# Performance work log

Hardware: AMD Instinct MI355X
Metric: run time of the kernel (lower is better)

## Reference

```python
import jax, jax.numpy as jnp
import numpy as np
import math

N_ENT = 200000
N_USERS = 100000
N_FACTORS = 4
N_REL = 26
CH = 64
N_EDGES = 1000000
NNZ = 1000000
KG_HEADS = 2


def scatter_softmax(scores, seg, num_segments):
    # numerically-stable softmax over groups defined by seg (per-head softmax)
    m = jax.ops.segment_max(scores, seg, num_segments=num_segments)
    m = jnp.where(jnp.isfinite(m), m, 0.0)
    e = jnp.exp(scores - m[seg])
    d = jax.ops.segment_sum(e, seg, num_segments=num_segments)
    return e / d[seg]


def setup_inputs() -> dict:
    key = jax.random.key(0)
    ks = jax.random.split(key, 11)
    return {
        "entity_emb": jax.random.normal(ks[0], (N_ENT, CH), dtype=jnp.float32) * 0.1,
        "user_emb": jax.random.normal(ks[1], (N_USERS, CH), dtype=jnp.float32) * 0.1,
        "latent_emb": jax.random.normal(ks[2], (N_FACTORS, CH), dtype=jnp.float32) * 0.1,
        "edge_index": jax.random.randint(ks[3], (2, N_EDGES), 0, N_ENT),
        "edge_type": jax.random.randint(ks[4], (N_EDGES,), 1, N_REL),  # in [1, N_REL-1]
        "ui_rows": jax.random.randint(ks[5], (NNZ,), 0, N_USERS),
        "ui_cols": jax.random.randint(ks[6], (NNZ,), 0, N_ENT),
        "ui_vals": jax.random.uniform(ks[7], (NNZ,), dtype=jnp.float32),
        "weight": jax.random.normal(ks[8], (N_REL - 1, CH), dtype=jnp.float32) * 0.1,
        "disen_weight_att": jax.random.normal(ks[9], (N_FACTORS, N_REL - 1), dtype=jnp.float32) * 0.1,
        "kg_W_r": jax.random.normal(ks[10], (CH, CH), dtype=jnp.float32) * (1.0 / math.sqrt(CH)),
    }


def reference(entity_emb, user_emb, latent_emb, edge_index, edge_type,
              ui_rows, ui_cols, ui_vals, weight, disen_weight_att, kg_W_r):
    head, tail = edge_index[0], edge_index[1]
    d_k = CH // KG_HEADS

    # --- Invariant_Capture.relation_aware_att ---
    rel_emb = weight[edge_type - 1]            # [E, C] gather
    h_emb = entity_emb[head]                   # [E, C] gather
    q = (h_emb @ kg_W_r).reshape(-1, KG_HEADS, d_k)
    k = (rel_emb @ kg_W_r).reshape(-1, KG_HEADS, d_k)
    score_r = ((q * k).sum(-1) / math.sqrt(d_k)).mean(-1)   # [E]
    rel_attn = scatter_softmax(score_r, head, N_ENT)

    # --- Invariant_Capture.kg_inv_capture ---
    t_emb = entity_emb[tail]                   # [E, C] gather
    r_emb = rel_emb * rel_attn[:, None]
    # bmm(cat(h,r), cat(t,r)^T) == h.t + r.r per edge
    score_trip = (h_emb * t_emb).sum(-1) + (r_emb * r_emb).sum(-1)
    kg_mask = scatter_softmax(score_trip, head, N_ENT)       # invariant_mask [E]

    # --- Aggregator: KG scatter-mean with invariant mask ---
    neigh = t_emb * rel_emb * kg_mask[:, None]               # [E, C]
    sums = jax.ops.segment_sum(neigh, head, num_segments=N_ENT)
    cnt = jax.ops.segment_sum(jnp.ones((neigh.shape[0],), dtype=neigh.dtype), head, num_segments=N_ENT)
    entity_agg = sums / jnp.maximum(cnt, 1.0)[:, None]       # scatter_mean

    # --- Aggregator: user side ---
    score = jax.nn.softmax(user_emb @ latent_emb.T, axis=1)  # [U, F]
    user_agg = jax.ops.segment_sum(entity_emb[ui_cols] * ui_vals[:, None], ui_rows, num_segments=N_USERS)
    disen_weight = jax.nn.softmax(disen_weight_att, axis=-1) @ weight  # [F, C]
    # (expand(U,F,C) * score[:,:,None]).sum(1) == score @ disen_weight
    user_agg = user_agg * (score @ disen_weight) + user_agg

    return jnp.concatenate([entity_agg, user_agg], axis=0)   # [N_ENT+N_USERS, C]
```

## Files before the change

kernel.cpp:

```cpp
#include <hip/hip_runtime.h>
#include <math.h>

#define N_ENT 200000
#define N_USERS 100000
#define NKEY 300000
#define N_FACTORS 4
#define NREL1 25
#define CH 64
#define N_EDGES 1000000
#define NNZ 1000000
#define NREC 2000000
#define BSHIFT 11
#define BKEYS 2048
#define NBUCKET 147
#define TILE 2048
#define NBLK_FILL ((NREC + TILE - 1) / TILE)
#define CAP 32768
#define NCONVB ((N_ENT * 8 + 1023) / 1024)

#define SCORE_SCALE 0.08838834764831845f
#define INV_Q14 6.103888176768602e-05f

typedef __attribute__((ext_vector_type(2))) float floatx2;

__device__ __forceinline__ float red8(float d) {
    d += __shfl_xor(d, 1);
    d += __shfl_xor(d, 2);
    d += __shfl_xor(d, 4);
    return d;
}
__device__ __forceinline__ float dot4(float4 a, float4 b) {
    return a.x * b.x + a.y * b.y + a.z * b.z + a.w * b.w;
}
__device__ __forceinline__ unsigned short f2bf(float f) {
    unsigned u = __float_as_uint(f);
    u += 0x7FFFu + ((u >> 16) & 1u);
    return (unsigned short)(u >> 16);
}
__device__ __forceinline__ float bf2f(unsigned short u) {
    return __uint_as_float(((unsigned)u) << 16);
}
__device__ __forceinline__ float4 bf4lo(uint4 t) {
    return make_float4(__uint_as_float(t.x << 16), __uint_as_float(t.x & 0xFFFF0000u),
                       __uint_as_float(t.y << 16), __uint_as_float(t.y & 0xFFFF0000u));
}
__device__ __forceinline__ float4 bf4hi(uint4 t) {
    return make_float4(__uint_as_float(t.z << 16), __uint_as_float(t.z & 0xFFFF0000u),
                       __uint_as_float(t.w << 16), __uint_as_float(t.w & 0xFFFF0000u));
}
__device__ __forceinline__ void fp8x8_dec(uint2 v, float4& lo, float4& hi) {
    floatx2 a = __builtin_amdgcn_cvt_pk_f32_fp8((int)v.x, false);
    floatx2 b = __builtin_amdgcn_cvt_pk_f32_fp8((int)v.x, true);
    floatx2 c = __builtin_amdgcn_cvt_pk_f32_fp8((int)v.y, false);
    floatx2 d = __builtin_amdgcn_cvt_pk_f32_fp8((int)v.y, true);
    lo = make_float4(a[0], a[1], b[0], b[1]);
    hi = make_float4(c[0], c[1], d[0], d[1]);
}
__device__ __forceinline__ uint2 fp8x8_enc(float4 lo, float4 hi) {
    int l = __builtin_amdgcn_cvt_pk_fp8_f32(lo.x, lo.y, 0, false);
    l = __builtin_amdgcn_cvt_pk_fp8_f32(lo.z, lo.w, l, true);
    int h = __builtin_amdgcn_cvt_pk_fp8_f32(hi.x, hi.y, 0, false);
    h = __builtin_amdgcn_cvt_pk_fp8_f32(hi.z, hi.w, h, true);
    return make_uint2((unsigned)l, (unsigned)h);
}

__device__ __forceinline__
void precompute_dev(int tid, unsigned char* shmraw,
                    const float* __restrict__ W,
                    const float* __restrict__ weight,
                    const float* __restrict__ datt,
                    float* __restrict__ Mvec,
                    float* __restrict__ wnorm,
                    float* __restrict__ disen) {
    float* sW   = (float*)shmraw;
    float* sw   = sW + 4096;
    float* sWWt = sw + 1600;
    for (int i = tid; i < 64 * 64; i += 256) sW[i] = W[i];
    for (int i = tid; i < NREL1 * 64; i += 256) sw[i] = weight[i];
    __syncthreads();
    for (int e = tid; e < 64 * 64; e += 256) {
        int i = e >> 6, j = e & 63;
        float s = 0.f;
        for (int k = 0; k < 64; ++k) s += sW[i * 64 + k] * sW[j * 64 + k];
        sWWt[e] = s;
    }
    __syncthreads();
    for (int e = tid; e < NREL1 * 64; e += 256) {
        int r = e >> 6, i = e & 63;
        float s = 0.f;
        for (int j = 0; j < 64; ++j) s += sWWt[i * 64 + j] * sw[r * 64 + j];
        Mvec[e] = s;
    }
    for (int r = tid; r < NREL1; r += 256) {
        float s = 0.f;
        for (int j = 0; j < 64; ++j) { float v = sw[r * 64 + j]; s += v * v; }
        wnorm[r] = s;
    }
    for (int e = tid; e < N_FACTORS * 64; e += 256) {
        int f = e >> 6, c = e & 63;
        float m = -1e30f;
        for (int r = 0; r < NREL1; ++r) m = fmaxf(m, datt[f * NREL1 + r]);
        float ssum = 0.f, acc = 0.f;
        for (int r = 0; r < NREL1; ++r) {
            float p = expf(datt[f * NREL1 + r] - m);
            ssum += p;
            acc += p * sw[r * 64 + c];
        }
        disen[e] = acc / ssum;
    }
}

__global__ void binpre_k(const int* __restrict__ head, const int* __restrict__ tail,
                         const int* __restrict__ etype,
                         const int* __restrict__ rows, const int* __restrict__ cols,
                         const float* __restrict__ vals,
                         unsigned* __restrict__ gcur,
                         uint2* __restrict__ stg,
                         const float* __restrict__ W,
                         const float* __restrict__ weight,
                         const float* __restrict__ datt,
                         float* __restrict__ Mvec,
                         float* __restrict__ wnorm,
                         float* __restrict__ disen) {
    __shared__ __align__(16) unsigned char shmraw[39936];
    int tid = threadIdx.x;
    if (blockIdx.x >= NBLK_FILL) {
        precompute_dev(tid, shmraw, W, weight, datt, Mvec, wnorm, disen);
        return;
    }
    unsigned* hist  = (unsigned*)shmraw;
    unsigned* base  = hist + 640;
    unsigned* gbase = base + 160;
    unsigned* wsum  = gbase + 160;
    uint2*    lrec  = (uint2*)(shmraw + 4096);

    int tile0 = blockIdx.x * TILE;
    int tile_n = min(TILE, NREC - tile0);
    for (int i = tid; i < 640; i += 256) hist[i] = 0u;
    __syncthreads();
    int wid = tid >> 6;
    unsigned key[8], pay[8], rank[8];
    for (int r = 0; r < 8; ++r) {
        int li = r * 256 + tid;
        key[r] = 0xFFFFFFFFu;
        if (li < tile_n) {
            int idx = tile0 + li;
            unsigned k, p;
            if (idx < N_EDGES) {
                k = (unsigned)head[idx];
                p = (unsigned)tail[idx] | ((unsigned)(etype[idx] - 1) << 18);
            } else {
                int j = idx - N_EDGES;
                k = (unsigned)(N_ENT + rows[j]);
                unsigned q = (unsigned)(vals[j] * 16383.f + 0.5f);
                p = (unsigned)cols[j] | (q << 18);
            }
            key[r] = k; pay[r] = p;
            rank[r] = atomicAdd(&hist[wid * 160 + (k >> BSHIFT)], 1u);
        }
    }
    __syncthreads();
    unsigned tot = 0;
    if (tid < NBUCKET) {
        unsigned h0 = hist[tid], h1 = hist[160 + tid];
        unsigned h2 = hist[320 + tid], h3 = hist[480 + tid];
        tot = h0 + h1 + h2 + h3;
        hist[tid] = 0u;
        hist[160 + tid] = h0;
        hist[320 + tid] = h0 + h1;
        hist[480 + tid] = h0 + h1 + h2;
    }
    unsigned v = tot;
    int lane = tid & 63;
    for (int o = 1; o < 64; o <<= 1) {
        unsigned t = __shfl_up(v, o);
        if (lane >= o) v += t;
    }
    if (lane == 63) wsum[wid] = v;
    __syncthreads();
    unsigned pre = 0;
    for (int w = 0; w < wid; ++w) pre += wsum[w];
    if (tid < NBUCKET) {
        base[tid] = pre + v - tot;
        gbase[tid] = (unsigned)tid * CAP + (tot ? atomicAdd(&gcur[tid], tot) : 0u);
    }
    __syncthreads();
    for (int r = 0; r < 8; ++r) {
        if (key[r] != 0xFFFFFFFFu) {
            unsigned b = key[r] >> BSHIFT;
            lrec[base[b] + hist[wid * 160 + b] + rank[r]] = make_uint2(key[r], pay[r]);
        }
    }
    __syncthreads();
    for (int i = tid; i < tile_n; i += 256) {
        uint2 rec = lrec[i];
        unsigned b = rec.x >> BSHIFT;
        unsigned dst = gbase[b] + ((unsigned)i - base[b]);
        if (dst < (b + 1u) * CAP) stg[dst] = rec;
    }
}

__device__ __forceinline__
void place_bucket_dev(int b, int tid, const uint2* __restrict__ stg,
                      const unsigned* __restrict__ gcur,
                      unsigned* __restrict__ offs, unsigned* __restrict__ csr,
                      unsigned* shm) {
    unsigned c = (tid < NBUCKET) ? gcur[tid] : 0u;
    if (c > CAP) c = CAP;
    if (tid < 256) shm[tid] = c;
    __syncthreads();
    for (int o = 1; o < 256; o <<= 1) {
        unsigned t = (tid >= o && tid < 256) ? shm[tid - o] : 0u;
        __syncthreads();
        if (tid < 256) shm[tid] += t;
        __syncthreads();
    }
    if (tid == 0) {
        unsigned cb = gcur[b]; if (cb > CAP) cb = CAP;
        shm[3073] = cb;
        shm[3072] = shm[b] - cb;
        if (b == NBUCKET - 1) offs[NKEY] = shm[NBUCKET - 1];
    }
    __syncthreads();
    unsigned n = shm[3073], gb = shm[3072];
    const uint2* seg = stg + (size_t)b * CAP;
    unsigned* cnt = shm;
    unsigned* sc  = shm + 2048;
    cnt[tid * 2] = 0u; cnt[tid * 2 + 1] = 0u;
    __syncthreads();
    for (unsigned i = tid; i < n; i += 1024) {
        unsigned kk = seg[i].x - ((unsigned)b << BSHIFT);
        atomicAdd(&cnt[kk], 1u);
    }
    __syncthreads();
    unsigned c0 = cnt[tid * 2], c1 = cnt[tid * 2 + 1];
    unsigned tsum = c0 + c1;
    sc[tid] = tsum; __syncthreads();
    for (int o = 1; o < 1024; o <<= 1) {
        unsigned t = (tid >= o) ? sc[tid - o] : 0u;
        __syncthreads();
        sc[tid] += t;
        __syncthreads();
    }
    unsigned e0 = sc[tid] - tsum;
    unsigned e1 = e0 + c0;
    int k0 = (b << BSHIFT) + tid * 2;
    if (k0 < NKEY)     offs[k0]     = gb + e0;
    if (k0 + 1 < NKEY) offs[k0 + 1] = gb + e1;
    cnt[tid * 2] = e0; cnt[tid * 2 + 1] = e1;
    __syncthreads();
    for (unsigned i = tid; i < n; i += 1024) {
        uint2 rec = seg[i];
        unsigned kk = rec.x - ((unsigned)b << BSHIFT);
        unsigned pos = atomicAdd(&cnt[kk], 1u);
        csr[gb + pos] = rec.y;
    }
}

template<bool W8>
__device__ __forceinline__
void convE_dev(int cb, int tid, const float* __restrict__ ent,
               const float* __restrict__ Mvec,
               uint4* __restrict__ entb, unsigned short* __restrict__ E16,
               uint2* __restrict__ ent8, unsigned* shm) {
    float4* sM = (float4*)shm;
    for (int i = tid; i < NREL1 * 16; i += 1024) sM[i] = ((const float4*)Mvec)[i];
    __syncthreads();
    int idx = cb * 1024 + tid;
    int h = idx >> 3;
    int sub = tid & 7;
    if (h >= N_ENT) return;
    const float4* e4 = (const float4*)ent;
    float4 a = e4[h * 16 + sub * 2], b4 = e4[h * 16 + sub * 2 + 1];
    uint4 o;
    o.x = (unsigned)f2bf(a.x)  | ((unsigned)f2bf(a.y)  << 16);
    o.y = (unsigned)f2bf(a.z)  | ((unsigned)f2bf(a.w)  << 16);
    o.z = (unsigned)f2bf(b4.x) | ((unsigned)f2bf(b4.y) << 16);
    o.w = (unsigned)f2bf(b4.z) | ((unsigned)f2bf(b4.w) << 16);
    entb[h * 8 + sub] = o;
    if (W8) ent8[h * 8 + sub] = fp8x8_enc(a, b4);
    for (int r = 0; r < NREL1; ++r) {
        float d = dot4(a, sM[r * 16 + sub * 2]) + dot4(b4, sM[r * 16 + sub * 2 + 1]);
        d = red8(d);
        if (sub == (r & 7)) E16[h * NREL1 + r] = f2bf(__expf(d * SCORE_SCALE));
    }
}

template<bool W8>
__global__ void placeconv_k(const uint2* __restrict__ stg,
                            const unsigned* __restrict__ gcur,
                            unsigned* __restrict__ offs,
                            unsigned* __restrict__ csr,
                            const float* __restrict__ ent,
                            const float* __restrict__ Mvec,
                            uint4* __restrict__ entb,
                            unsigned short* __restrict__ E16,
                            uint2* __restrict__ ent8) {
    __shared__ __align__(16) unsigned shm[3074];
    int b = blockIdx.x;
    if (b < NBUCKET)
        place_bucket_dev(b, threadIdx.x, stg, gcur, offs, csr, shm);
    else
        convE_dev<W8>(b - NBUCKET, threadIdx.x, ent, Mvec, entb, E16, ent8, shm);
}

__global__ void binplace3_k(const uint2* __restrict__ stg,
                            const unsigned* __restrict__ gcur,
                            unsigned* __restrict__ offs,
                            unsigned* __restrict__ csr) {
    __shared__ __align__(16) unsigned shm[3074];
    place_bucket_dev(blockIdx.x, threadIdx.x, stg, gcur, offs, csr, shm);
}

template<int MODE>
__device__ __forceinline__
void ent_row(const uint4* entb, const uint2* ent8, const float4* e4,
             int t, int sub, float4& lo, float4& hi) {
    if (MODE == 2) {
        fp8x8_dec(ent8[t * 8 + sub], lo, hi);
    } else if (MODE == 1) {
        uint4 tb = entb[t * 8 + sub];
        lo = bf4lo(tb); hi = bf4hi(tb);
    } else {
        lo = e4[t * 16 + sub * 2]; hi = e4[t * 16 + sub * 2 + 1];
    }
}

template<int MODE>
__global__ void gather8_k(const float* __restrict__ ent,
                          const uint4* __restrict__ entb,
                          const uint2* __restrict__ ent8,
                          const unsigned short* __restrict__ E16,
                          const float* __restrict__ weight,
                          const float* __restrict__ Mvec,
                          const float* __restrict__ wnorm,
                          const float* __restrict__ uemb,
                          const float* __restrict__ lat,
                          const float* __restrict__ disen,
                          const unsigned* __restrict__ offs,
                          const unsigned* __restrict__ csr,
                          float* __restrict__ out) {
    int gid = blockIdx.x * 256 + threadIdx.x;
    int key = gid >> 3;
    int sub = threadIdx.x & 7;
    if (key >= NKEY) return;
    unsigned beg = offs[key], end = offs[key + 1];
    const float4* e4 = (const float4*)ent;
    const float4* w4 = (const float4*)weight;
    float4* o4 = (float4*)out;
    const float4 z = make_float4(0.f, 0.f, 0.f, 0.f);

    if (key < N_ENT) {
        int h = key;
        if (beg == end) {
            o4[h * 16 + sub * 2] = z;
            o4[h * 16 + sub * 2 + 1] = z;
            return;
        }
        float4 hv0, hv1;
        ent_row<MODE>(entb, ent8, e4, h, sub, hv0, hv1);
        float dr = 0.f;
        if (MODE > 0) {
            for (unsigned i = beg + sub; i < end; i += 8)
                dr += bf2f(E16[h * NREL1 + (csr[i] >> 18)]);
            dr = red8(dr);
        } else {
            for (unsigned i = beg; i < end; ++i) {
                int r = csr[i] >> 18;
                float d = dot4(hv0, ((const float4*)Mvec)[r * 16 + sub * 2]) +
                          dot4(hv1, ((const float4*)Mvec)[r * 16 + sub * 2 + 1]);
                dr += __expf(red8(d) * SCORE_SCALE);
            }
        }
        float inv_dr = 1.0f / dr;
        float4 a0 = z, a1 = z;
        float dt = 0.f;
        unsigned i = beg;
        for (; i + 2 <= end; i += 2) {
            unsigned p0 = csr[i], p1 = csr[i + 1];
            int t0 = p0 & 0x3FFFF, r0 = p0 >> 18;
            int t1 = p1 & 0x3FFFF, r1 = p1 >> 18;
            float4 tv00, tv01, tv10, tv11;
            ent_row<MODE>(entb, ent8, e4, t0, sub, tv00, tv01);
            ent_row<MODE>(entb, ent8, e4, t1, sub, tv10, tv11);
            float d0 = red8(dot4(hv0, tv00) + dot4(hv1, tv01));
            float d1 = red8(dot4(hv0, tv10) + dot4(hv1, tv11));
            float er0, er1;
            if (MODE > 0) {
                er0 = bf2f(E16[h * NREL1 + r0]);
                er1 = bf2f(E16[h * NREL1 + r1]);
            } else {
                float q0 = dot4(hv0, ((const float4*)Mvec)[r0 * 16 + sub * 2]) +
                           dot4(hv1, ((const float4*)Mvec)[r0 * 16 + sub * 2 + 1]);
                float q1 = dot4(hv0, ((const float4*)Mvec)[r1 * 16 + sub * 2]) +
                           dot4(hv1, ((const float4*)Mvec)[r1 * 16 + sub * 2 + 1]);
                er0 = __expf(red8(q0) * SCORE_SCALE);
                er1 = __expf(red8(q1) * SCORE_SCALE);
            }
            float ra0 = er0 * inv_dr, ra1 = er1 * inv_dr;
            float et0 = __expf(d0 + ra0 * ra0 * wnorm[r0]);
            float et1 = __expf(d1 + ra1 * ra1 * wnorm[r1]);
            dt += et0 + et1;
            float4 wv;
            wv = w4[r0 * 16 + sub * 2];
            a0.x += et0 * tv00.x * wv.x; a0.y += et0 * tv00.y * wv.y;
            a0.z += et0 * tv00.z * wv.z; a0.w += et0 * tv00.w * wv.w;
            wv = w4[r0 * 16 + sub * 2 + 1];
            a1.x += et0 * tv01.x * wv.x; a1.y += et0 * tv01.y * wv.y;
            a1.z += et0 * tv01.z * wv.z; a1.w += et0 * tv01.w * wv.w;
            wv = w4[r1 * 16 + sub * 2];
            a0.x += et1 * tv10.x * wv.x; a0.y += et1 * tv10.y * wv.y;
            a0.z += et1 * tv10.z * wv.z; a0.w += et1 * tv10.w * wv.w;
            wv = w4[r1 * 16 + sub * 2 + 1];
            a1.x += et1 * tv11.x * wv.x; a1.y += et1 * tv11.y * wv.y;
            a1.z += et1 * tv11.z * wv.z; a1.w += et1 * tv11.w * wv.w;
        }
        if (i < end) {
            unsigned p = csr[i];
            int t = p & 0x3FFFF, r = p >> 18;
            float4 tv0, tv1;
            ent_row<MODE>(entb, ent8, e4, t, sub, tv0, tv1);
            float d = red8(dot4(hv0, tv0) + dot4(hv1, tv1));
            float er;
            if (MODE > 0) {
                er = bf2f(E16[h * NREL1 + r]);
            } else {
                float q = dot4(hv0, ((const float4*)Mvec)[r * 16 + sub * 2]) +
                          dot4(hv1, ((const float4*)Mvec)[r * 16 + sub * 2 + 1]);
                er = __expf(red8(q) * SCORE_SCALE);
            }
            float ra = er * inv_dr;
            float et = __expf(d + ra * ra * wnorm[r]);
            dt += et;
            float4 wv;
            wv = w4[r * 16 + sub * 2];
            a0.x += et * tv0.x * wv.x; a0.y += et * tv0.y * wv.y;
            a0.z += et * tv0.z * wv.z; a0.w += et * tv0.w * wv.w;
            wv = w4[r * 16 + sub * 2 + 1];
            a1.x += et * tv1.x * wv.x; a1.y += et * tv1.y * wv.y;
            a1.z += et * tv1.z * wv.z; a1.w += et * tv1.w * wv.w;
        }
        float inv = 1.0f / (dt * (float)(end - beg));
        a0.x *= inv; a0.y *= inv; a0.z *= inv; a0.w *= inv;
        a1.x *= inv; a1.y *= inv; a1.z *= inv; a1.w *= inv;
        o4[h * 16 + sub * 2] = a0;
        o4[h * 16 + sub * 2 + 1] = a1;
    } else {
        int u = key - N_ENT;
        float4 a0 = z, a1 = z;
        unsigned i = beg;
        for (; i + 2 <= end; i += 2) {
            unsigned p0 = csr[i], p1 = csr[i + 1];
            int c0 = p0 & 0x3FFFF, c1 = p1 & 0x3FFFF;
            float v0 = (float)(p0 >> 18) * INV_Q14;
            float v1 = (float)(p1 >> 18) * INV_Q14;
            float4 tv00, tv01, tv10, tv11;
            ent_row<(MODE > 0 ? 1 : 0)>(entb, ent8, e4, c0, sub, tv00, tv01);
            ent_row<(MODE > 0 ? 1 : 0)>(entb, ent8, e4, c1, sub, tv10, tv11);
            a0.x += v0 * tv00.x + v1 * tv10.x; a0.y += v0 * tv00.y + v1 * tv10.y;
            a0.z += v0 * tv00.z + v1 * tv10.z; a0.w += v0 * tv00.w + v1 * tv10.w;
            a1.x += v0 * tv01.x + v1 * tv11.x; a1.y += v0 * tv01.y + v1 * tv11.y;
            a1.z += v0 * tv01.z + v1 * tv11.z; a1.w += v0 * tv01.w + v1 * tv11.w;
        }
        if (i < end) {
            unsigned p = csr[i];
            int c = p & 0x3FFFF;
            float v = (float)(p >> 18) * INV_Q14;
            float4 tv0, tv1;
            ent_row<(MODE > 0 ? 1 : 0)>(entb, ent8, e4, c, sub, tv0, tv1);
            a0.x += v * tv0.x; a0.y += v * tv0.y; a0.z += v * tv0.z; a0.w += v * tv0.w;
            a1.x += v * tv1.x; a1.y += v * tv1.y; a1.z += v * tv1.z; a1.w += v * tv1.w;
        }
        float4 uv0 = ((const float4*)uemb)[u * 16 + sub * 2];
        float4 uv1 = ((const float4*)uemb)[u * 16 + sub * 2 + 1];
        float d[N_FACTORS];
        for (int f = 0; f < N_FACTORS; ++f) {
            float t = dot4(uv0, ((const float4*)lat)[f * 16 + sub * 2]) +
                      dot4(uv1, ((const float4*)lat)[f * 16 + sub * 2 + 1]);
            d[f] = red8(t);
        }
        float m = fmaxf(fmaxf(d[0], d[1]), fmaxf(d[2], d[3]));
        float s = 0.f, p_[N_FACTORS];
        for (int f = 0; f < N_FACTORS; ++f) { p_[f] = __expf(d[f] - m); s += p_[f]; }
        float invs = 1.0f / s;
        float4 g0 = z, g1 = z;
        for (int f = 0; f < N_FACTORS; ++f) {
            float w = p_[f] * invs;
            float4 dv = ((const float4*)disen)[f * 16 + sub * 2];
            g0.x += w * dv.x; g0.y += w * dv.y; g0.z += w * dv.z; g0.w += w * dv.w;
            dv = ((const float4*)disen)[f * 16 + sub * 2 + 1];
            g1.x += w * dv.x; g1.y += w * dv.y; g1.z += w * dv.z; g1.w += w * dv.w;
        }
        a0.x *= (1.0f + g0.x); a0.y *= (1.0f + g0.y);
        a0.z *= (1.0f + g0.z); a0.w *= (1.0f + g0.w);
        a1.x *= (1.0f + g1.x); a1.y *= (1.0f + g1.y);
        a1.z *= (1.0f + g1.z); a1.w *= (1.0f + g1.w);
        o4[key * 16 + sub * 2] = a0;
        o4[key * 16 + sub * 2 + 1] = a1;
    }
}

extern "C" void kernel_launch(void* const* d_in, const int* in_sizes, int n_in,
                              void* d_out, int out_size, void* d_ws, size_t ws_size,
                              hipStream_t stream) {
    (void)in_sizes; (void)n_in; (void)out_size;
    const float* ent    = (const float*)d_in[0];
    const float* uemb   = (const float*)d_in[1];
    const float* lat    = (const float*)d_in[2];
    const int*   eidx   = (const int*)d_in[3];
    const int*   etype  = (const int*)d_in[4];
    const int*   urows  = (const int*)d_in[5];
    const int*   ucols  = (const int*)d_in[6];
    const float* uvals  = (const float*)d_in[7];
    const float* weight = (const float*)d_in[8];
    const float* datt   = (const float*)d_in[9];
    const float* W      = (const float*)d_in[10];

    const int* head = eidx;
    const int* tail = eidx + N_EDGES;
    float* out = (float*)d_out;

    uint2* stg = (uint2*)d_out;

    unsigned* gcur  = (unsigned*)d_ws;
    unsigned* offs  = gcur + 256;
    float*    Mvec  = (float*)(offs + NKEY + 2);
    float*    wnorm = Mvec + NREL1 * 64;
    float*    disen = wnorm + 32;
    unsigned* csr   = (unsigned*)(disen + N_FACTORS * 64);
    unsigned* entw  = csr + NREC;
    uint4*    entb  = (uint4*)entw;
    unsigned short* E16 = (unsigned short*)(entw + (size_t)N_ENT * 32);
    uint2*    ent8  = (uint2*)(entw + (size_t)N_ENT * 32 +
                               ((size_t)N_ENT * NREL1 + 1) / 2);

    size_t base_words = 256 + (NKEY + 2) + 1888 + (size_t)NREC;
    size_t need1 = (base_words + 8900000ull) * 4;
    size_t need2 = (base_words + 12100000ull) * 4;
    size_t need_out = (size_t)NBUCKET * CAP * 8;
    int mode = (ws_size >= need2) ? 2 : (ws_size >= need1) ? 1 : 0;
    if (ws_size < base_words * 4 || (size_t)out_size * 4 < need_out) return;

    const int BLK = 256;

    hipMemsetAsync(gcur, 0, 256 * sizeof(unsigned), stream);
    binpre_k<<<NBLK_FILL + 1, BLK, 0, stream>>>(
        head, tail, etype, urows, ucols, uvals, gcur, stg,
        W, weight, datt, Mvec, wnorm, disen);

    if (mode == 2) {
        placeconv_k<true><<<NBUCKET + NCONVB, 1024, 0, stream>>>(
            stg, gcur, offs, csr, ent, Mvec, entb, E16, ent8);
    } else if (mode == 1) {
        placeconv_k<false><<<NBUCKET + NCONVB, 1024, 0, stream>>>(
            stg, gcur, offs, csr, ent, Mvec, entb, E16, ent8);
    } else {
        binplace3_k<<<NBUCKET, 1024, 0, stream>>>(stg, gcur, offs, csr);
    }

    int gridG = (NKEY * 8 + BLK - 1) / BLK;
    if (mode == 2) {
        gather8_k<2><<<gridG, BLK, 0, stream>>>(
            ent, entb, ent8, E16, weight, Mvec, wnorm,
            uemb, lat, disen, offs, csr, out);
    } else if (mode == 1) {
        gather8_k<1><<<gridG, BLK, 0, stream>>>(
            ent, entb, ent8, E16, weight, Mvec, wnorm,
            uemb, lat, disen, offs, csr, out);
    } else {
        gather8_k<0><<<gridG, BLK, 0, stream>>>(
            ent, entb, ent8, E16, weight, Mvec, wnorm,
            uemb, lat, disen, offs, csr, out);
    }
}
```

Before: 196.1 us.

## Move entity bf16/fp8 table conversion into binning kernel, keep E16 in place pass

Splits the fused entity conversion so the bf16 and fp8 table writes run as extra blocks of the first binning kernel, which does not depend on Mvec. The second kernel now only computes the per-relation exp scores (E16) by reading the bf16 table rather than the fp32 embeddings. This balances work across the two launches and shrinks the second kernel's read traffic. In exchange, E16 is computed from bf16-rounded embeddings instead of fp32, which adds a small precision change, and the first launch gets many more blocks.

```diff
diff --git a/kernel.cpp b/kernel.cpp
--- a/kernel.cpp
+++ b/kernel.cpp
@@ -16,7 +16,8 @@
 #define TILE 2048
 #define NBLK_FILL ((NREC + TILE - 1) / TILE)
 #define CAP 32768
-#define NCONVB ((N_ENT * 8 + 1023) / 1024)
+#define NCONVB ((N_ENT * 8 + 255) / 256)
+#define NE16B  ((N_ENT * 8 + 1023) / 1024)
 
 #define SCORE_SCALE 0.08838834764831845f
 #define INV_Q14 6.103888176768602e-05f
@@ -110,6 +111,26 @@
     }
 }
 
+template<bool W8>
+__device__ __forceinline__
+void convtbl_dev(int cb, int tid, const float* __restrict__ ent,
+                 uint4* __restrict__ entb, uint2* __restrict__ ent8) {
+    int idx = cb * 256 + tid;
+    int h = idx >> 3;
+    int sub = idx & 7;
+    if (h >= N_ENT) return;
+    const float4* e4 = (const float4*)ent;
+    float4 a = e4[h * 16 + sub * 2], b4 = e4[h * 16 + sub * 2 + 1];
+    uint4 o;
+    o.x = (unsigned)f2bf(a.x)  | ((unsigned)f2bf(a.y)  << 16);
+    o.y = (unsigned)f2bf(a.z)  | ((unsigned)f2bf(a.w)  << 16);
+    o.z = (unsigned)f2bf(b4.x) | ((unsigned)f2bf(b4.y) << 16);
+    o.w = (unsigned)f2bf(b4.z) | ((unsigned)f2bf(b4.w) << 16);
+    entb[h * 8 + sub] = o;
+    if (W8) ent8[h * 8 + sub] = fp8x8_enc(a, b4);
+}
+
+template<bool W8>
 __global__ void binpre_k(const int* __restrict__ head, const int* __restrict__ tail,
                          const int* __restrict__ etype,
                          const int* __restrict__ rows, const int* __restrict__ cols,
@@ -121,11 +142,18 @@
                          const float* __restrict__ datt,
                          float* __restrict__ Mvec,
                          float* __restrict__ wnorm,
-                         float* __restrict__ disen) {
+                         float* __restrict__ disen,
+                         const float* __restrict__ ent,
+                         uint4* __restrict__ entb,
+                         uint2* __restrict__ ent8) {
     __shared__ __align__(16) unsigned char shmraw[39936];
     int tid = threadIdx.x;
-    if (blockIdx.x >= NBLK_FILL) {
+    if (blockIdx.x == NBLK_FILL) {
         precompute_dev(tid, shmraw, W, weight, datt, Mvec, wnorm, disen);
+        return;
+    }
+    if (blockIdx.x > NBLK_FILL) {
+        convtbl_dev<W8>(blockIdx.x - NBLK_FILL - 1, tid, ent, entb, ent8);
         return;
     }
     unsigned* hist  = (unsigned*)shmraw;
@@ -257,12 +285,10 @@
     }
 }
 
-template<bool W8>
 __device__ __forceinline__
-void convE_dev(int cb, int tid, const float* __restrict__ ent,
-               const float* __restrict__ Mvec,
-               uint4* __restrict__ entb, unsigned short* __restrict__ E16,
-               uint2* __restrict__ ent8, unsigned* shm) {
+void e16_dev(int cb, int tid, const uint4* __restrict__ entb,
+             const float* __restrict__ Mvec,
+             unsigned short* __restrict__ E16, unsigned* shm) {
     float4* sM = (float4*)shm;
     for (int i = tid; i < NREL1 * 16; i += 1024) sM[i] = ((const float4*)Mvec)[i];
     __syncthreads();
@@ -270,15 +296,8 @@
     int h = idx >> 3;
     int sub = tid & 7;
     if (h >= N_ENT) return;
-    const float4* e4 = (const float4*)ent;
-    float4 a = e4[h * 16 + sub * 2], b4 = e4[h * 16 + sub * 2 + 1];
-    uint4 o;
-    o.x = (unsigned)f2bf(a.x)  | ((unsigned)f2bf(a.y)  << 16);
-    o.y = (unsigned)f2bf(a.z)  | ((unsigned)f2bf(a.w)  << 16);
-    o.z = (unsigned)f2bf(b4.x) | ((unsigned)f2bf(b4.y) << 16);
-    o.w = (unsigned)f2bf(b4.z) | ((unsigned)f2bf(b4.w) << 16);
-    entb[h * 8 + sub] = o;
-    if (W8) ent8[h * 8 + sub] = fp8x8_enc(a, b4);
+    uint4 tb = entb[h * 8 + sub];
+    float4 a = bf4lo(tb), b4 = bf4hi(tb);
     for (int r = 0; r < NREL1; ++r) {
         float d = dot4(a, sM[r * 16 + sub * 2]) + dot4(b4, sM[r * 16 + sub * 2 + 1]);
         d = red8(d);
@@ -286,22 +305,19 @@
     }
 }
 
-template<bool W8>
-__global__ void placeconv_k(const uint2* __restrict__ stg,
-                            const unsigned* __restrict__ gcur,
-                            unsigned* __restrict__ offs,
-                            unsigned* __restrict__ csr,
-                            const float* __restrict__ ent,
-                            const float* __restrict__ Mvec,
-                            uint4* __restrict__ entb,
-                            unsigned short* __restrict__ E16,
-                            uint2* __restrict__ ent8) {
+__global__ void placee16_k(const uint2* __restrict__ stg,
+                           const unsigned* __restrict__ gcur,
+                           unsigned* __restrict__ offs,
+                           unsigned* __restrict__ csr,
+                           const uint4* __restrict__ entb,
+                           const float* __restrict__ Mvec,
+                           unsigned short* __restrict__ E16) {
     __shared__ __align__(16) unsigned shm[3074];
     int b = blockIdx.x;
     if (b < NBUCKET)
         place_bucket_dev(b, threadIdx.x, stg, gcur, offs, csr, shm);
     else
-        convE_dev<W8>(b - NBUCKET, threadIdx.x, ent, Mvec, entb, E16, ent8, shm);
+        e16_dev(b - NBUCKET, threadIdx.x, entb, Mvec, E16, shm);
 }
 
 __global__ void binplace3_k(const uint2* __restrict__ stg,
@@ -542,18 +558,22 @@
     if (ws_size < base_words * 4 || (size_t)out_size * 4 < need_out) return;
 
     const int BLK = 256;
+    int gridPre = NBLK_FILL + 1 + (mode >= 1 ? NCONVB : 0);
 
     hipMemsetAsync(gcur, 0, 256 * sizeof(unsigned), stream);
-    binpre_k<<<NBLK_FILL + 1, BLK, 0, stream>>>(
-        head, tail, etype, urows, ucols, uvals, gcur, stg,
-        W, weight, datt, Mvec, wnorm, disen);
-
     if (mode == 2) {
-        placeconv_k<true><<<NBUCKET + NCONVB, 1024, 0, stream>>>(
-            stg, gcur, offs, csr, ent, Mvec, entb, E16, ent8);
-    } else if (mode == 1) {
-        placeconv_k<false><<<NBUCKET + NCONVB, 1024, 0, stream>>>(
-            stg, gcur, offs, csr, ent, Mvec, entb, E16, ent8);
+        binpre_k<true><<<gridPre, BLK, 0, stream>>>(
+            head, tail, etype, urows, ucols, uvals, gcur, stg,
+            W, weight, datt, Mvec, wnorm, disen, ent, entb, ent8);
+    } else {
+        binpre_k<false><<<gridPre, BLK, 0, stream>>>(
+            head, tail, etype, urows, ucols, uvals, gcur, stg,
+            W, weight, datt, Mvec, wnorm, disen, ent, entb, ent8);
+    }
+
+    if (mode >= 1) {
+        placee16_k<<<NBUCKET + NE16B, 1024, 0, stream>>>(
+            stg, gcur, offs, csr, entb, Mvec, E16);
     } else {
         binplace3_k<<<NBUCKET, 1024, 0, stream>>>(stg, gcur, offs, csr);
     }
```

Result: faster. 191.4 us (-2.4%).
